# Kernel optimization log

Hardware: AMD Instinct MI355X
Metric: run time of the kernel (lower is better)

The kernel has to match this reference:

```python
import jax, jax.numpy as jnp
import numpy as np

EPSILON = 0.01  # from init_kwargs

def setup_inputs() -> dict:
    key = jax.random.key(0)
    k1, k2, k3, k4 = jax.random.split(key, 4)
    N, E, D = 100000, 3200000, 4
    x = jax.random.normal(k1, (N, D), dtype=jnp.float32)
    edge_index = jax.random.randint(k2, (2, E), 0, N, dtype=jnp.int32)
    boo_values = jax.random.normal(k3, (E, D, D), dtype=jnp.float32)
    mask = jnp.ones((N, 1), dtype=jnp.float32)
    diag = jax.random.uniform(k4, (N, D), dtype=jnp.float32)
    return {"x": x, "edge_index": edge_index, "boo_values": boo_values,
            "mask": mask, "diag": diag}

def reference(x, edge_index, boo_values, mask, diag):
    # y = eps*diag*x + A @ (diag * (A^T @ x)), A blocked-sparse with
    # per-edge blocks A_{row,col} = boo_values[e] in R^{DxD}.
    N = x.shape[0]
    row, col = edge_index[0], edge_index[1]
    # spmv_t (A^T x): gather x at row i, message A_ij^T x_i, scatter-add to col j
    msg_t = jnp.einsum('eji,ej->ei', boo_values, x[row])  # [E, D]
    AT_x = jax.ops.segment_sum(msg_t, col, num_segments=N) * mask  # [N, D]
    eps_x = EPSILON * x
    AT_x = AT_x * diag
    eps_x = eps_x * diag
    # spmv (A v): gather v at col j, message A_ij v_j, scatter-add to row i
    msg = jnp.einsum('eij,ej->ei', boo_values, AT_x[col])  # [E, D]
    A_AT_x = jax.ops.segment_sum(msg, row, num_segments=N) * mask  # [N, D]
    return eps_x + A_AT_x
```

## Files before the change

### kernel.cpp

```cpp
#include <hip/hip_runtime.h>

#define EPSILON 0.01f

#define BLK    256
#define SLICE  2048
#define SLOG   11
#define PCH    26
#define BCH    2048
#define MAXS   64


__global__ void init_cursors(int* cur1, int* cur2, int S, int cap) {
    int t = threadIdx.x;
    if (t < S) { cur1[t] = t * cap; cur2[t] = t * cap; }
}

__global__ void __launch_bounds__(BLK) bin_kernel(
    const int* __restrict__ row, const int* __restrict__ col,
    int2* __restrict__ bins1, int2* __restrict__ bins2,
    int* __restrict__ cur1, int* __restrict__ cur2,
    long long E, int S)
{
    __shared__ int h1[MAXS], h2[MAXS], b1[MAXS], b2[MAXS];
    const int t = threadIdx.x;
    if (t < S) { h1[t] = 0; h2[t] = 0; }
    __syncthreads();

    long long start = (long long)blockIdx.x * BCH;
    long long end   = start + BCH; if (end > E) end = E;

    for (long long t0 = start + (long long)t * 4; t0 < end; t0 += (long long)BLK * 4) {
        if (t0 + 4 <= end) {
            int4 c = *reinterpret_cast<const int4*>(col + t0);
            int4 r = *reinterpret_cast<const int4*>(row + t0);
            atomicAdd(&h1[c.x >> SLOG], 1); atomicAdd(&h1[c.y >> SLOG], 1);
            atomicAdd(&h1[c.z >> SLOG], 1); atomicAdd(&h1[c.w >> SLOG], 1);
            atomicAdd(&h2[r.x >> SLOG], 1); atomicAdd(&h2[r.y >> SLOG], 1);
            atomicAdd(&h2[r.z >> SLOG], 1); atomicAdd(&h2[r.w >> SLOG], 1);
        } else {
            for (long long e = t0; e < end; ++e) {
                atomicAdd(&h1[col[e] >> SLOG], 1);
                atomicAdd(&h2[row[e] >> SLOG], 1);
            }
        }
    }
    __syncthreads();
    if (t < S) {
        b1[t] = atomicAdd(&cur1[t], h1[t]); h1[t] = 0;
        b2[t] = atomicAdd(&cur2[t], h2[t]); h2[t] = 0;
    }
    __syncthreads();

    for (long long t0 = start + (long long)t * 4; t0 < end; t0 += (long long)BLK * 4) {
        long long lim4 = (t0 + 4 <= end) ? t0 + 4 : end;
        if (t0 + 4 <= end) {
            int4 c = *reinterpret_cast<const int4*>(col + t0);
            int4 r = *reinterpret_cast<const int4*>(row + t0);
            int cc[4] = {c.x, c.y, c.z, c.w};
            int rr[4] = {r.x, r.y, r.z, r.w};
            #pragma unroll
            for (int u = 0; u < 4; ++u) {
                int s1 = cc[u] >> SLOG;
                int i1 = b1[s1] + atomicAdd(&h1[s1], 1);
                bins1[i1] = make_int2((int)(t0 + u), ((cc[u] & (SLICE - 1)) << 17) | rr[u]);
                int s2 = rr[u] >> SLOG;
                int i2 = b2[s2] + atomicAdd(&h2[s2], 1);
                bins2[i2] = make_int2((int)(t0 + u), ((rr[u] & (SLICE - 1)) << 17) | cc[u]);
            }
        } else {
            for (long long e = t0; e < lim4; ++e) {
                int cv = col[e], rv = row[e];
                int s1 = cv >> SLOG;
                int i1 = b1[s1] + atomicAdd(&h1[s1], 1);
                bins1[i1] = make_int2((int)e, ((cv & (SLICE - 1)) << 17) | rv);
                int s2 = rv >> SLOG;
                int i2 = b2[s2] + atomicAdd(&h2[s2], 1);
                bins2[i2] = make_int2((int)e, ((rv & (SLICE - 1)) << 17) | cv);
            }
        }
    }
}

template<int PASS, int STAGED>
__global__ void __launch_bounds__(BLK) pass_kernel(
    const float4* __restrict__ boo,
    const int2*   __restrict__ bins,
    const int*    __restrict__ cur,
    const float4* __restrict__ src,
    const float*  __restrict__ mask,
    float*        __restrict__ dst,
    int N, int cap, int P)
{
    __shared__ float acc[SLICE * 4];

    const int s    = blockIdx.x / P;
    const int p    = blockIdx.x - s * P;
    const int base = s << SLOG;
    const int lim  = min(SLICE, N - base);

    for (int i = threadIdx.x; i < SLICE * 4; i += BLK) acc[i] = 0.0f;
    __syncthreads();

    const int cnt = cur[s] - s * cap;
    const int lo  = (int)((long long)cnt * p / P);
    const int hi  = (int)((long long)cnt * (p + 1) / P);
    const int2* __restrict__ bin = bins + (size_t)s * cap;

    for (int i = lo + (int)threadIdx.x; i < hi; i += BLK) {
        int2 rec = bin[i];
        const float4* B = boo + (long long)rec.x * 4;
        float4 b0 = B[0], b1 = B[1], b2 = B[2], b3 = B[3];
        float4 v = src[rec.y & 0x1FFFF];
        float* a = acc + (((unsigned)rec.y) >> 17) * 4;
        if (PASS == 1) {
            atomicAdd(a + 0, b0.x*v.x + b1.x*v.y + b2.x*v.z + b3.x*v.w);
            atomicAdd(a + 1, b0.y*v.x + b1.y*v.y + b2.y*v.z + b3.y*v.w);
            atomicAdd(a + 2, b0.z*v.x + b1.z*v.y + b2.z*v.z + b3.z*v.w);
            atomicAdd(a + 3, b0.w*v.x + b1.w*v.y + b2.w*v.z + b3.w*v.w);
        } else {
            atomicAdd(a + 0, b0.x*v.x + b0.y*v.y + b0.z*v.z + b0.w*v.w);
            atomicAdd(a + 1, b1.x*v.x + b1.y*v.y + b1.z*v.z + b1.w*v.w);
            atomicAdd(a + 2, b2.x*v.x + b2.y*v.y + b2.z*v.z + b2.w*v.w);
            atomicAdd(a + 3, b3.x*v.x + b3.y*v.y + b3.z*v.z + b3.w*v.w);
        }
    }
    __syncthreads();

    if (STAGED) {
        float* st = dst + (size_t)blockIdx.x * (SLICE * 4);
        for (int f = threadIdx.x; f < lim * 4; f += BLK) st[f] = acc[f];
    } else if (PASS == 1) {
        for (int f = threadIdx.x; f < lim * 4; f += BLK)
            unsafeAtomicAdd(dst + ((long long)base * 4 + f), acc[f]);
    } else {
        for (int f = threadIdx.x; f < lim * 4; f += BLK) {
            float mv = mask[base + (f >> 2)];
            unsafeAtomicAdd(dst + ((long long)base * 4 + f), acc[f] * mv);
        }
    }
}

__global__ void __launch_bounds__(BLK) mid_staged_kernel(
    const float4* __restrict__ stage,
    const float4* __restrict__ d4,
    const float*  __restrict__ mask,
    float4* __restrict__ v4,
    int N, int P)
{
    int n = blockIdx.x * BLK + threadIdx.x;
    if (n >= N) return;
    int s = n >> SLOG, local = n & (SLICE - 1);
    const float4* t = stage + ((size_t)s * P) * SLICE + local;
    float4 a = make_float4(0.f, 0.f, 0.f, 0.f);
    for (int p = 0; p < P; ++p) {
        float4 u = t[(size_t)p * SLICE];
        a.x += u.x; a.y += u.y; a.z += u.z; a.w += u.w;
    }
    float4 dv = d4[n];
    float  m  = mask[n];
    a.x *= dv.x * m; a.y *= dv.y * m; a.z *= dv.z * m; a.w *= dv.w * m;
    v4[n] = a;
}

__global__ void __launch_bounds__(BLK) fin_staged_kernel(
    const float4* __restrict__ stage,
    const float4* __restrict__ x4,
    const float4* __restrict__ d4,
    const float*  __restrict__ mask,
    float4* __restrict__ out4,
    int N, int P)
{
    int n = blockIdx.x * BLK + threadIdx.x;
    if (n >= N) return;
    int s = n >> SLOG, local = n & (SLICE - 1);
    const float4* t = stage + ((size_t)s * P) * SLICE + local;
    float4 a = make_float4(0.f, 0.f, 0.f, 0.f);
    for (int p = 0; p < P; ++p) {
        float4 u = t[(size_t)p * SLICE];
        a.x += u.x; a.y += u.y; a.z += u.z; a.w += u.w;
    }
    float4 xv = x4[n];
    float4 dv = d4[n];
    float  m  = mask[n];
    float4 o;
    o.x = EPSILON * xv.x * dv.x + a.x * m;
    o.y = EPSILON * xv.y * dv.y + a.y * m;
    o.z = EPSILON * xv.z * dv.z + a.z * m;
    o.w = EPSILON * xv.w * dv.w + a.w * m;
    out4[n] = o;
}

__global__ void __launch_bounds__(BLK) mid_atomic_kernel(
    const float4* __restrict__ x4,
    const float4* __restrict__ d4,
    const float*  __restrict__ mask,
    float4* __restrict__ atx,
    float4* __restrict__ out4,
    int N)
{
    int n = blockIdx.x * BLK + threadIdx.x;
    if (n >= N) return;
    float4 a  = atx[n];
    float4 dv = d4[n];
    float  m  = mask[n];
    a.x *= dv.x * m; a.y *= dv.y * m; a.z *= dv.z * m; a.w *= dv.w * m;
    atx[n] = a;
    float4 xv = x4[n];
    float4 o;
    o.x = EPSILON * xv.x * dv.x; o.y = EPSILON * xv.y * dv.y;
    o.z = EPSILON * xv.z * dv.z; o.w = EPSILON * xv.w * dv.w;
    out4[n] = o;
}

__global__ void __launch_bounds__(256) spmvt_kernel(
    const float4* __restrict__ boo, const int* __restrict__ row,
    const int* __restrict__ col, const float* __restrict__ x,
    float* __restrict__ ATx, long long E)
{
    long long t = (long long)blockIdx.x * blockDim.x + threadIdx.x;
    long long e = t >> 2;
    int j = (int)(t & 3);
    if (e >= E) return;
    float4 b = boo[e * 4 + j];
    int r = row[e];
    float xj = x[r * 4 + j];
    float4 p;
    p.x = b.x * xj; p.y = b.y * xj; p.z = b.z * xj; p.w = b.w * xj;
    p.x += __shfl_xor(p.x, 1); p.y += __shfl_xor(p.y, 1);
    p.z += __shfl_xor(p.z, 1); p.w += __shfl_xor(p.w, 1);
    p.x += __shfl_xor(p.x, 2); p.y += __shfl_xor(p.y, 2);
    p.z += __shfl_xor(p.z, 2); p.w += __shfl_xor(p.w, 2);
    float v = (j == 0) ? p.x : (j == 1) ? p.y : (j == 2) ? p.z : p.w;
    int c = col[e];
    unsafeAtomicAdd(&ATx[c * 4 + j], v);
}

__global__ void __launch_bounds__(256) spmv_kernel(
    const float4* __restrict__ boo, const int* __restrict__ row,
    const int* __restrict__ col, const float* __restrict__ vv,
    const float* __restrict__ mask, float* __restrict__ out, long long E)
{
    long long t = (long long)blockIdx.x * blockDim.x + threadIdx.x;
    long long e = t >> 2;
    int i = (int)(t & 3);
    if (e >= E) return;
    float4 b = boo[e * 4 + i];
    int c = col[e];
    const float4* v4 = (const float4*)vv;
    float4 v = v4[c];
    float mi = b.x * v.x + b.y * v.y + b.z * v.z + b.w * v.w;
    int r = row[e];
    float mr = mask[r];
    unsafeAtomicAdd(&out[r * 4 + i], mi * mr);
}

extern "C" void kernel_launch(void* const* d_in, const int* in_sizes, int n_in,
                              void* d_out, int out_size, void* d_ws, size_t ws_size,
                              hipStream_t stream) {
    const float* x    = (const float*)d_in[0];
    const int*   ei   = (const int*)d_in[1];
    const float* boo  = (const float*)d_in[2];
    const float* mask = (const float*)d_in[3];
    const float* diag = (const float*)d_in[4];
    float* out = (float*)d_out;

    int N = in_sizes[0] / 4;
    long long E = in_sizes[1] / 2;
    const int* row = ei;
    const int* col = ei + E;

    int S = (N + SLICE - 1) >> SLOG;
    int cap = (int)((E + S - 1) / S);
    cap += cap * 3 / 10;
    cap = (cap + 255) & ~255;

    size_t o_v   = 0;
    size_t o_cur = ((size_t)N * 16 + 255) & ~(size_t)255;
    size_t o_b1  = o_cur + 1024;
    size_t szb   = (size_t)S * cap * 8;
    size_t o_b2  = o_b1 + szb;
    size_t o_st  = o_b2 + szb;
    size_t szst  = (size_t)S * PCH * SLICE * 16;

    bool ok   = (S <= MAXS) && (N <= (1 << 17)) && ((E & 3) == 0 || true);
    int  tier = (!ok) ? 3 : (ws_size >= o_st + szst) ? 1
                          : (ws_size >= o_st)        ? 2 : 3;

    float* v     = (float*)((char*)d_ws + o_v);
    int*   cur1  = (int*)((char*)d_ws + o_cur);
    int*   cur2  = cur1 + 128;
    int2*  bins1 = (int2*)((char*)d_ws + o_b1);
    int2*  bins2 = (int2*)((char*)d_ws + o_b2);
    float* stage = (float*)((char*)d_ws + o_st);

    const int gNode = (N + BLK - 1) / BLK;
    const int gBin  = (int)((E + BCH - 1) / BCH);
    const int gPass = S * PCH;

    if (tier <= 2) {
        init_cursors<<<1, MAXS, 0, stream>>>(cur1, cur2, S, cap);
        bin_kernel<<<gBin, BLK, 0, stream>>>(row, col, bins1, bins2, cur1, cur2, E, S);
        if (tier == 1) {
            pass_kernel<1, 1><<<gPass, BLK, 0, stream>>>(
                (const float4*)boo, bins1, cur1, (const float4*)x, mask, stage, N, cap, PCH);
            mid_staged_kernel<<<gNode, BLK, 0, stream>>>(
                (const float4*)stage, (const float4*)diag, mask, (float4*)v, N, PCH);
            pass_kernel<2, 1><<<gPass, BLK, 0, stream>>>(
                (const float4*)boo, bins2, cur2, (const float4*)v, mask, stage, N, cap, PCH);
            fin_staged_kernel<<<gNode, BLK, 0, stream>>>(
                (const float4*)stage, (const float4*)x, (const float4*)diag, mask,
                (float4*)out, N, PCH);
        } else {
            hipMemsetAsync(v, 0, (size_t)N * 16, stream);
            pass_kernel<1, 0><<<gPass, BLK, 0, stream>>>(
                (const float4*)boo, bins1, cur1, (const float4*)x, mask, v, N, cap, PCH);
            mid_atomic_kernel<<<gNode, BLK, 0, stream>>>(
                (const float4*)x, (const float4*)diag, mask, (float4*)v, (float4*)out, N);
            pass_kernel<2, 0><<<gPass, BLK, 0, stream>>>(
                (const float4*)boo, bins2, cur2, (const float4*)v, mask, out, N, cap, PCH);
        }
    } else {
        hipMemsetAsync(v, 0, (size_t)N * 16, stream);
        long long T = E * 4;
        int gEdge = (int)((T + BLK - 1) / BLK);
        spmvt_kernel<<<gEdge, BLK, 0, stream>>>(
            (const float4*)boo, row, col, x, v, E);
        mid_atomic_kernel<<<gNode, BLK, 0, stream>>>(
            (const float4*)x, (const float4*)diag, mask, (float4*)v, (float4*)out, N);
        spmv_kernel<<<gEdge, BLK, 0, stream>>>(
            (const float4*)boo, row, col, v, mask, out, E);
    }
}
```

Measured before the change: 544.4 us.

## Stage binning through shared memory and split edge blocks across four lanes

The bin kernel now sorts each chunk of edges by slice in shared memory and then writes them to global bins contiguously, one side at a time, in place of scattering each record straight to global memory. The pass kernel assigns four lanes per edge, each loading one float4 row of the 4x4 block, which makes block loads coalesced. Pass 1 reduces its transposed product with wave shuffles, and two edges are in flight per iteration. The slice size is halved and the chunk and partition counts change, which raises the slice count and the shared-memory footprint per block.

```diff
diff --git a/kernel.cpp b/kernel.cpp
--- a/kernel.cpp
+++ b/kernel.cpp
@@ -3,11 +3,11 @@
 #define EPSILON 0.01f
 
 #define BLK    256
-#define SLICE  2048
-#define SLOG   11
-#define PCH    26
-#define BCH    2048
-#define MAXS   64
+#define SLICE  1024
+#define SLOG   10
+#define PCH    20
+#define BCH    4096
+#define MAXS   128
 
 
 __global__ void init_cursors(int* cur1, int* cur2, int S, int cap) {
@@ -21,63 +21,77 @@
     int* __restrict__ cur1, int* __restrict__ cur2,
     long long E, int S)
 {
-    __shared__ int h1[MAXS], h2[MAXS], b1[MAXS], b2[MAXS];
+    __shared__ int2 st[BCH];
+    __shared__ unsigned char ss[BCH];
+    __shared__ int hist[MAXS], rnk[MAXS], sbase[MAXS], gbase[MAXS];
     const int t = threadIdx.x;
-    if (t < S) { h1[t] = 0; h2[t] = 0; }
-    __syncthreads();
 
     long long start = (long long)blockIdx.x * BCH;
-    long long end   = start + BCH; if (end > E) end = E;
-
-    for (long long t0 = start + (long long)t * 4; t0 < end; t0 += (long long)BLK * 4) {
-        if (t0 + 4 <= end) {
-            int4 c = *reinterpret_cast<const int4*>(col + t0);
-            int4 r = *reinterpret_cast<const int4*>(row + t0);
-            atomicAdd(&h1[c.x >> SLOG], 1); atomicAdd(&h1[c.y >> SLOG], 1);
-            atomicAdd(&h1[c.z >> SLOG], 1); atomicAdd(&h1[c.w >> SLOG], 1);
-            atomicAdd(&h2[r.x >> SLOG], 1); atomicAdd(&h2[r.y >> SLOG], 1);
-            atomicAdd(&h2[r.z >> SLOG], 1); atomicAdd(&h2[r.w >> SLOG], 1);
-        } else {
-            for (long long e = t0; e < end; ++e) {
-                atomicAdd(&h1[col[e] >> SLOG], 1);
-                atomicAdd(&h2[row[e] >> SLOG], 1);
+    long long endl  = start + BCH; if (endl > E) endl = E;
+    const int cnt = (int)(endl - start);
+
+    for (int side = 0; side < 2; ++side) {
+        const int* __restrict__ key = side ? row : col;
+        const int* __restrict__ oth = side ? col : row;
+        int2* __restrict__ bins = side ? bins2 : bins1;
+        int*  __restrict__ cur  = side ? cur2  : cur1;
+
+        if (t < MAXS) { hist[t] = 0; rnk[t] = 0; }
+        __syncthreads();
+
+        for (int i0 = t * 4; i0 < cnt; i0 += BLK * 4) {
+            if (i0 + 4 <= cnt) {
+                int4 k = *reinterpret_cast<const int4*>(key + start + i0);
+                atomicAdd(&hist[k.x >> SLOG], 1);
+                atomicAdd(&hist[k.y >> SLOG], 1);
+                atomicAdd(&hist[k.z >> SLOG], 1);
+                atomicAdd(&hist[k.w >> SLOG], 1);
+            } else {
+                for (int i = i0; i < cnt; ++i)
+                    atomicAdd(&hist[key[start + i] >> SLOG], 1);
             }
         }
-    }
-    __syncthreads();
-    if (t < S) {
-        b1[t] = atomicAdd(&cur1[t], h1[t]); h1[t] = 0;
-        b2[t] = atomicAdd(&cur2[t], h2[t]); h2[t] = 0;
-    }
-    __syncthreads();
-
-    for (long long t0 = start + (long long)t * 4; t0 < end; t0 += (long long)BLK * 4) {
-        long long lim4 = (t0 + 4 <= end) ? t0 + 4 : end;
-        if (t0 + 4 <= end) {
-            int4 c = *reinterpret_cast<const int4*>(col + t0);
-            int4 r = *reinterpret_cast<const int4*>(row + t0);
-            int cc[4] = {c.x, c.y, c.z, c.w};
-            int rr[4] = {r.x, r.y, r.z, r.w};
-            #pragma unroll
-            for (int u = 0; u < 4; ++u) {
-                int s1 = cc[u] >> SLOG;
-                int i1 = b1[s1] + atomicAdd(&h1[s1], 1);
-                bins1[i1] = make_int2((int)(t0 + u), ((cc[u] & (SLICE - 1)) << 17) | rr[u]);
-                int s2 = rr[u] >> SLOG;
-                int i2 = b2[s2] + atomicAdd(&h2[s2], 1);
-                bins2[i2] = make_int2((int)(t0 + u), ((rr[u] & (SLICE - 1)) << 17) | cc[u]);
+        __syncthreads();
+
+        if (t == 0) {
+            int run = 0;
+            for (int s2 = 0; s2 < S; ++s2) { sbase[s2] = run; run += hist[s2]; }
+        }
+        if (t < S) gbase[t] = atomicAdd(&cur[t], hist[t]);
+        __syncthreads();
+
+        for (int i0 = t * 4; i0 < cnt; i0 += BLK * 4) {
+            if (i0 + 4 <= cnt) {
+                int4 k = *reinterpret_cast<const int4*>(key + start + i0);
+                int4 o = *reinterpret_cast<const int4*>(oth + start + i0);
+                int kk[4] = {k.x, k.y, k.z, k.w};
+                int oo[4] = {o.x, o.y, o.z, o.w};
+                #pragma unroll
+                for (int u = 0; u < 4; ++u) {
+                    int s2 = kk[u] >> SLOG;
+                    int slot = sbase[s2] + atomicAdd(&rnk[s2], 1);
+                    st[slot] = make_int2((int)(start + i0 + u),
+                                         ((kk[u] & (SLICE - 1)) << 17) | oo[u]);
+                    ss[slot] = (unsigned char)s2;
+                }
+            } else {
+                for (int i = i0; i < cnt; ++i) {
+                    int kv = key[start + i], ov = oth[start + i];
+                    int s2 = kv >> SLOG;
+                    int slot = sbase[s2] + atomicAdd(&rnk[s2], 1);
+                    st[slot] = make_int2((int)(start + i),
+                                         ((kv & (SLICE - 1)) << 17) | ov);
+                    ss[slot] = (unsigned char)s2;
+                }
             }
-        } else {
-            for (long long e = t0; e < lim4; ++e) {
-                int cv = col[e], rv = row[e];
-                int s1 = cv >> SLOG;
-                int i1 = b1[s1] + atomicAdd(&h1[s1], 1);
-                bins1[i1] = make_int2((int)e, ((cv & (SLICE - 1)) << 17) | rv);
-                int s2 = rv >> SLOG;
-                int i2 = b2[s2] + atomicAdd(&h2[s2], 1);
-                bins2[i2] = make_int2((int)e, ((rv & (SLICE - 1)) << 17) | cv);
-            }
-        }
+        }
+        __syncthreads();
+
+        for (int i = t; i < cnt; i += BLK) {
+            int s2 = ss[i];
+            bins[(size_t)gbase[s2] + (i - sbase[s2])] = st[i];
+        }
+        __syncthreads();
     }
 }
 
@@ -106,29 +120,47 @@
     const int hi  = (int)((long long)cnt * (p + 1) / P);
     const int2* __restrict__ bin = bins + (size_t)s * cap;
 
-    for (int i = lo + (int)threadIdx.x; i < hi; i += BLK) {
-        int2 rec = bin[i];
-        const float4* B = boo + (long long)rec.x * 4;
-        float4 b0 = B[0], b1 = B[1], b2 = B[2], b3 = B[3];
+    const int j  = (int)(threadIdx.x & 3);
+    const int g0 = (int)(threadIdx.x >> 2);
+
+    auto process = [&](int2 rec, float4 b) {
         float4 v = src[rec.y & 0x1FFFF];
-        float* a = acc + (((unsigned)rec.y) >> 17) * 4;
-        if (PASS == 1) {
-            atomicAdd(a + 0, b0.x*v.x + b1.x*v.y + b2.x*v.z + b3.x*v.w);
-            atomicAdd(a + 1, b0.y*v.x + b1.y*v.y + b2.y*v.z + b3.y*v.w);
-            atomicAdd(a + 2, b0.z*v.x + b1.z*v.y + b2.z*v.z + b3.z*v.w);
-            atomicAdd(a + 3, b0.w*v.x + b1.w*v.y + b2.w*v.z + b3.w*v.w);
+        int loc = ((unsigned)rec.y) >> 17;
+        float val;
+        if (PASS == 2) {
+            val = b.x * v.x + b.y * v.y + b.z * v.z + b.w * v.w;
         } else {
-            atomicAdd(a + 0, b0.x*v.x + b0.y*v.y + b0.z*v.z + b0.w*v.w);
-            atomicAdd(a + 1, b1.x*v.x + b1.y*v.y + b1.z*v.z + b1.w*v.w);
-            atomicAdd(a + 2, b2.x*v.x + b2.y*v.y + b2.z*v.z + b2.w*v.w);
-            atomicAdd(a + 3, b3.x*v.x + b3.y*v.y + b3.z*v.z + b3.w*v.w);
-        }
+            float xj = (j == 0) ? v.x : (j == 1) ? v.y : (j == 2) ? v.z : v.w;
+            float4 q;
+            q.x = b.x * xj; q.y = b.y * xj; q.z = b.z * xj; q.w = b.w * xj;
+            q.x += __shfl_xor(q.x, 1); q.y += __shfl_xor(q.y, 1);
+            q.z += __shfl_xor(q.z, 1); q.w += __shfl_xor(q.w, 1);
+            q.x += __shfl_xor(q.x, 2); q.y += __shfl_xor(q.y, 2);
+            q.z += __shfl_xor(q.z, 2); q.w += __shfl_xor(q.w, 2);
+            val = (j == 0) ? q.x : (j == 1) ? q.y : (j == 2) ? q.z : q.w;
+        }
+        atomicAdd(&acc[loc * 4 + j], val);
+    };
+
+    int i = lo + g0;
+    for (; i + 64 < hi; i += 128) {
+        int2 ra = bin[i];
+        int2 rb = bin[i + 64];
+        float4 ba = boo[(long long)ra.x * 4 + j];
+        float4 bb = boo[(long long)rb.x * 4 + j];
+        process(ra, ba);
+        process(rb, bb);
+    }
+    if (i < hi) {
+        int2 ra = bin[i];
+        float4 ba = boo[(long long)ra.x * 4 + j];
+        process(ra, ba);
     }
     __syncthreads();
 
     if (STAGED) {
-        float* st = dst + (size_t)blockIdx.x * (SLICE * 4);
-        for (int f = threadIdx.x; f < lim * 4; f += BLK) st[f] = acc[f];
+        float* stg = dst + (size_t)blockIdx.x * (SLICE * 4);
+        for (int f = threadIdx.x; f < lim * 4; f += BLK) stg[f] = acc[f];
     } else if (PASS == 1) {
         for (int f = threadIdx.x; f < lim * 4; f += BLK)
             unsafeAtomicAdd(dst + ((long long)base * 4 + f), acc[f]);
@@ -276,19 +308,19 @@
 
     size_t o_v   = 0;
     size_t o_cur = ((size_t)N * 16 + 255) & ~(size_t)255;
-    size_t o_b1  = o_cur + 1024;
+    size_t o_b1  = o_cur + 2048;
     size_t szb   = (size_t)S * cap * 8;
     size_t o_b2  = o_b1 + szb;
     size_t o_st  = o_b2 + szb;
     size_t szst  = (size_t)S * PCH * SLICE * 16;
 
-    bool ok   = (S <= MAXS) && (N <= (1 << 17)) && ((E & 3) == 0 || true);
+    bool ok   = (S <= MAXS) && (N <= (1 << 17));
     int  tier = (!ok) ? 3 : (ws_size >= o_st + szst) ? 1
                           : (ws_size >= o_st)        ? 2 : 3;
 
     float* v     = (float*)((char*)d_ws + o_v);
     int*   cur1  = (int*)((char*)d_ws + o_cur);
-    int*   cur2  = cur1 + 128;
+    int*   cur2  = cur1 + 256;
     int2*  bins1 = (int2*)((char*)d_ws + o_b1);
     int2*  bins2 = (int2*)((char*)d_ws + o_b2);
     float* stage = (float*)((char*)d_ws + o_st);
```

Result: faster. 508.6 us (-6.6%).
